# Optimization experiments

Measured on AMD Instinct MI355X. Metric: run time of the kernel, lower is better.

The kernel has to match this reference:

```python
import jax, jax.numpy as jnp
import numpy as np

# XORChainModel.forward: state[0] = inputs[0]; state[i] = state[i-1] ^ inputs[i]
# i.e. a cumulative XOR (inclusive prefix scan with XOR) along the chain axis.
# XOR is associative, so we use jax.lax.associative_scan (log-depth parallel scan).

SEQ_LEN = 4096  # number of steps in the XOR chain (len(inputs) list in torch)
BITS = 8192     # self.bits: width of each bit vector


def setup_inputs() -> dict:
    key = jax.random.key(0)
    # inputs[i] is a 1-D bit vector of length BITS; stack the whole list into [S, BITS]
    inputs = jax.random.randint(key, (SEQ_LEN, BITS), 0, 2, dtype=jnp.int32)
    return {"inputs": inputs}


def reference(inputs):
    # outputs[i] = inputs[0] ^ inputs[1] ^ ... ^ inputs[i]
    # Equivalent to the torch module's list of per-step states, stacked on axis 0.
    return jax.lax.associative_scan(jnp.bitwise_xor, inputs, axis=0)
```

## Files before the change

kernel.cpp:

```cpp
#include <hip/hip_runtime.h>


#define S 4096
#define B 8192
#define B4 (B / 4)
#define CHUNK 32
#define NCHUNK (S / CHUNK)
#define TPB 256
#define NCOLTILE (B4 / TPB)

typedef unsigned int v4u __attribute__((ext_vector_type(4)));

__global__ __launch_bounds__(TPB) void xor_chunk_total(
        const v4u* __restrict__ in, v4u* __restrict__ ws) {
    const int colg  = blockIdx.x * TPB + threadIdx.x;
    const int chunk = blockIdx.y;
    const v4u* p = in + (size_t)chunk * CHUNK * B4 + colg;
    v4u acc = (v4u){0u, 0u, 0u, 0u};
#pragma unroll 16
    for (int r = 0; r < CHUNK; ++r) {
        acc ^= p[(size_t)r * B4];
    }
    ws[(size_t)chunk * B4 + colg] = acc;
}

#define K2_TPB 64
__global__ __launch_bounds__(K2_TPB) void xor_prefix_chunks(v4u* __restrict__ ws) {
    const int colg = blockIdx.x * K2_TPB + threadIdx.x;
    v4u acc = (v4u){0u, 0u, 0u, 0u};
    for (int b = 0; b < NCHUNK / 8; ++b) {
        v4u vals[8];
#pragma unroll
        for (int j = 0; j < 8; ++j) {
            vals[j] = ws[(size_t)(b * 8 + j) * B4 + colg];
        }
#pragma unroll
        for (int j = 0; j < 8; ++j) {
            v4u t = vals[j];
            ws[(size_t)(b * 8 + j) * B4 + colg] = acc;
            acc ^= t;
        }
    }
}

__global__ __launch_bounds__(TPB) void xor_scan_out(
        const v4u* __restrict__ in, const v4u* __restrict__ ws,
        v4u* __restrict__ out) {
    const int colg  = blockIdx.x * TPB + threadIdx.x;
    const int chunk = blockIdx.y;
    v4u acc = ws[(size_t)chunk * B4 + colg];
    const v4u* p = in  + (size_t)chunk * CHUNK * B4 + colg;
    v4u*       q = out + (size_t)chunk * CHUNK * B4 + colg;
#pragma unroll 16
    for (int r = 0; r < CHUNK; ++r) {
        acc ^= __builtin_nontemporal_load(&p[(size_t)r * B4]);
        __builtin_nontemporal_store(acc, &q[(size_t)r * B4]);
    }
}

extern "C" void kernel_launch(void* const* d_in, const int* in_sizes, int n_in,
                              void* d_out, int out_size, void* d_ws, size_t ws_size,
                              hipStream_t stream) {
    const v4u* in = (const v4u*)d_in[0];
    v4u* out = (v4u*)d_out;
    v4u* ws  = (v4u*)d_ws;

    dim3 grid1(NCOLTILE, NCHUNK);
    dim3 grid2(B4 / K2_TPB);
    xor_chunk_total<<<grid1, TPB, 0, stream>>>(in, ws);
    xor_prefix_chunks<<<grid2, K2_TPB, 0, stream>>>(ws);
    xor_scan_out<<<grid1, TPB, 0, stream>>>(in, ws, out);
}
```

Before: 255.7 us.

## Drop chunk-prefix kernel; each scan block XORs preceding chunk totals itself

Removes the middle sequential kernel that turned chunk totals into exclusive prefixes. Each block of the output kernel now XORs all earlier chunk totals directly, trading a launch and a serial pass for redundant reads of the small workspace, which should mostly hit in cache. Blocks are issued in reverse chunk order so the longest prefix loops start first, and input loads switch from nontemporal to regular so the second read of the input may hit in cache. Redundant workspace traffic grows quadratically with chunk count.

```diff
diff --git a/kernel.cpp b/kernel.cpp
--- a/kernel.cpp
+++ b/kernel.cpp
@@ -2,12 +2,11 @@
 
 
 #define S 4096
-#define B 8192
-#define B4 (B / 4)
+#define B4 2048
 #define CHUNK 32
 #define NCHUNK (S / CHUNK)
 #define TPB 256
-#define NCOLTILE (B4 / TPB)
+#define NCT (B4 / TPB)
 
 typedef unsigned int v4u __attribute__((ext_vector_type(4)));
 
@@ -24,36 +23,24 @@
     ws[(size_t)chunk * B4 + colg] = acc;
 }
 
-#define K2_TPB 64
-__global__ __launch_bounds__(K2_TPB) void xor_prefix_chunks(v4u* __restrict__ ws) {
-    const int colg = blockIdx.x * K2_TPB + threadIdx.x;
-    v4u acc = (v4u){0u, 0u, 0u, 0u};
-    for (int b = 0; b < NCHUNK / 8; ++b) {
-        v4u vals[8];
-#pragma unroll
-        for (int j = 0; j < 8; ++j) {
-            vals[j] = ws[(size_t)(b * 8 + j) * B4 + colg];
-        }
-#pragma unroll
-        for (int j = 0; j < 8; ++j) {
-            v4u t = vals[j];
-            ws[(size_t)(b * 8 + j) * B4 + colg] = acc;
-            acc ^= t;
-        }
-    }
-}
-
 __global__ __launch_bounds__(TPB) void xor_scan_out(
         const v4u* __restrict__ in, const v4u* __restrict__ ws,
         v4u* __restrict__ out) {
     const int colg  = blockIdx.x * TPB + threadIdx.x;
-    const int chunk = blockIdx.y;
-    v4u acc = ws[(size_t)chunk * B4 + colg];
+    const int chunk = (NCHUNK - 1) - blockIdx.y;
+
+    v4u excl = (v4u){0u, 0u, 0u, 0u};
+#pragma unroll 8
+    for (int c = 0; c < chunk; ++c) {
+        excl ^= ws[(size_t)c * B4 + colg];
+    }
+
     const v4u* p = in  + (size_t)chunk * CHUNK * B4 + colg;
     v4u*       q = out + (size_t)chunk * CHUNK * B4 + colg;
-#pragma unroll 16
+    v4u acc = excl;
+#pragma unroll 8
     for (int r = 0; r < CHUNK; ++r) {
-        acc ^= __builtin_nontemporal_load(&p[(size_t)r * B4]);
+        acc ^= p[(size_t)r * B4];
         __builtin_nontemporal_store(acc, &q[(size_t)r * B4]);
     }
 }
@@ -65,9 +52,7 @@
     v4u* out = (v4u*)d_out;
     v4u* ws  = (v4u*)d_ws;
 
-    dim3 grid1(NCOLTILE, NCHUNK);
-    dim3 grid2(B4 / K2_TPB);
-    xor_chunk_total<<<grid1, TPB, 0, stream>>>(in, ws);
-    xor_prefix_chunks<<<grid2, K2_TPB, 0, stream>>>(ws);
-    xor_scan_out<<<grid1, TPB, 0, stream>>>(in, ws, out);
+    dim3 grid(NCT, NCHUNK);
+    xor_chunk_total<<<grid, TPB, 0, stream>>>(in, ws);
+    xor_scan_out<<<grid, TPB, 0, stream>>>(in, ws, out);
 }
```

Result: faster. 247.3 us (-3.3%).
